# Kernel tuning notes

Measured on AMD Instinct MI355X. Metric: run time of the kernel, lower is better.

## Reference

```python
import jax, jax.numpy as jnp
import numpy as np

B, C, H, W = 8, 512, 64, 64
D = C // 8  # 64

def setup_inputs() -> dict:
    key = jax.random.key(0)
    ks = jax.random.split(key, 10)
    s = 0.02
    return {
        "x":  jax.random.normal(ks[0], (B, C, H, W), dtype=jnp.float32),
        "Wq": jax.random.normal(ks[1], (D, C), dtype=jnp.float32) * s,
        "bq": jnp.zeros((D,), dtype=jnp.float32),
        "Wk": jax.random.normal(ks[2], (D, C), dtype=jnp.float32) * s,
        "bk": jnp.zeros((D,), dtype=jnp.float32),
        "Wv": jax.random.normal(ks[3], (D, C), dtype=jnp.float32) * s,
        "bv": jnp.zeros((D,), dtype=jnp.float32),
        "Wo": jax.random.normal(ks[4], (C, D), dtype=jnp.float32) * s,
        "bo": jnp.zeros((C,), dtype=jnp.float32),
        "gamma": jnp.full((1,), 0.5, dtype=jnp.float32),
    }

def reference(x, Wq, bq, Wk, bk, Wv, bv, Wo, bo, gamma):
    b, c, h, w = x.shape
    n = h * w
    xf = x.reshape(b, c, n)                                   # (B, C, N)
    # 1x1 convs == channel matmuls (spectral_norm only reparametrizes the weight)
    q = jnp.einsum('dc,bcn->bnd', Wq, xf) + bq                # (B, N, D)
    k = jnp.einsum('dc,bcn->bdn', Wk, xf) + bk[:, None]       # (B, D, N)
    v = jnp.einsum('dc,bcn->bdn', Wv, xf) + bv[:, None]       # (B, D, N)
    # unscaled scores, softmax over key index (last dim)
    attn = jax.nn.softmax(jnp.einsum('bnd,bdm->bnm', q, k), axis=-1)  # (B, N, N)
    out = jnp.einsum('bdm,bnm->bdn', v, attn)                 # (B, D, N)
    out = jnp.einsum('cd,bdn->bcn', Wo, out) + bo[:, None]    # (B, C, N)
    return (out * gamma + xf).reshape(b, c, h, w)
```

## Files before the change

### kernel.cpp

```cpp
#include <hip/hip_runtime.h>
#include <hip/hip_bf16.h>

#define DEVFN __device__ __forceinline__

typedef __bf16 bf16x8 __attribute__((ext_vector_type(8)));
typedef float f32x4 __attribute__((ext_vector_type(4)));
typedef float float4_t __attribute__((ext_vector_type(4)));
typedef unsigned short ushort8_t __attribute__((ext_vector_type(8)));
typedef unsigned short ushort4_t __attribute__((ext_vector_type(4)));
typedef unsigned int uint4_t __attribute__((ext_vector_type(4)));

constexpr int Bd = 8, Cd = 512, Nd = 4096, Dd = 64;

DEVFN unsigned short f2bf(float f) {
    union { float f; unsigned int u; } v; v.f = f;
    unsigned int r = (v.u + 0x7FFFu + ((v.u >> 16) & 1u)) >> 16;
    return (unsigned short)r;
}

DEVFN unsigned int pack2(float a, float b) {
    __hip_bfloat162 h = __float22bfloat162_rn(make_float2(a, b));
    union { __hip_bfloat162 h; unsigned int u; } c; c.h = h;
    return c.u;
}

DEVFN bf16x8 ld_bf8(const unsigned short* p) {
    ushort8_t u = *(const ushort8_t*)p;
    return __builtin_bit_cast(bf16x8, u);
}

DEVFN f32x4 mfma16(bf16x8 a, bf16x8 b, f32x4 c) {
    return __builtin_amdgcn_mfma_f32_16x16x32_bf16(a, b, c, 0, 0, 0);
}

__global__ __launch_bounds__(256) void k_cvtw(
    const float* __restrict__ Wq, const float* __restrict__ Wk,
    const float* __restrict__ Wv, const float* __restrict__ Wo,
    unsigned short* __restrict__ w4)
{
    int i = blockIdx.x * 256 + threadIdx.x;
    w4[i]          = f2bf(Wq[i]);
    w4[32768 + i]  = f2bf(Wk[i]);
    w4[65536 + i]  = f2bf(Wv[i]);
    w4[98304 + i]  = f2bf(Wo[i]);
}

__global__ __launch_bounds__(256) void k_qkv(
    const float* __restrict__ x,
    const unsigned short* __restrict__ wq,
    const unsigned short* __restrict__ wk,
    const unsigned short* __restrict__ wv,
    const float* __restrict__ bq, const float* __restrict__ bk, const float* __restrict__ bv,
    unsigned short* __restrict__ q_nd, unsigned short* __restrict__ k_nd,
    unsigned short* __restrict__ v_dn)
{
    const int b   = blockIdx.y;
    const int n0  = blockIdx.x * 64;
    const int tid = threadIdx.x, wid = tid >> 6, l = tid & 63;
    const int lo  = l & 15, hi = l >> 4;
    const int n0w = n0 + wid * 16;
    const float* xb = x + (size_t)b * Cd * Nd;

    __shared__ unsigned short t_lds[4][16][72];
    __shared__ unsigned short vt_s[64][72];

    f32x4 accq[4] = {}, acck[4] = {}, accv[4] = {};

    for (int c0 = 0; c0 < Cd; c0 += 32) {
        ushort8_t ux;
        #pragma unroll
        for (int j = 0; j < 8; ++j)
            ux[j] = f2bf(xb[(size_t)(c0 + hi * 8 + j) * Nd + n0w + lo]);
        bf16x8 bx = __builtin_bit_cast(bf16x8, ux);
        #pragma unroll
        for (int ds = 0; ds < 4; ++ds) {
            const int wrow = (ds * 16 + lo) * Cd + c0 + hi * 8;
            accq[ds] = mfma16(ld_bf8(wq + wrow), bx, accq[ds]);
            acck[ds] = mfma16(ld_bf8(wk + wrow), bx, acck[ds]);
            accv[ds] = mfma16(ld_bf8(wv + wrow), bx, accv[ds]);
        }
    }

    const int row = l >> 2, dg = l & 3;

    #pragma unroll
    for (int ds = 0; ds < 4; ++ds) {
        ushort4_t u4;
        #pragma unroll
        for (int r = 0; r < 4; ++r) u4[r] = f2bf(accq[ds][r] + bq[ds*16 + hi*4 + r]);
        *(ushort4_t*)&t_lds[wid][lo][ds*16 + hi*4] = u4;
    }
    __syncthreads();
    {
        ushort8_t a0 = *(const ushort8_t*)&t_lds[wid][row][dg*16];
        ushort8_t a1 = *(const ushort8_t*)&t_lds[wid][row][dg*16 + 8];
        unsigned short* dst = q_nd + ((size_t)b * Nd + n0 + wid*16 + row) * 64 + dg*16;
        *(ushort8_t*)dst = a0; *(ushort8_t*)(dst + 8) = a1;
    }
    __syncthreads();

    #pragma unroll
    for (int ds = 0; ds < 4; ++ds) {
        ushort4_t u4;
        #pragma unroll
        for (int r = 0; r < 4; ++r) u4[r] = f2bf(acck[ds][r] + bk[ds*16 + hi*4 + r]);
        *(ushort4_t*)&t_lds[wid][lo][ds*16 + hi*4] = u4;
    }
    __syncthreads();
    {
        ushort8_t a0 = *(const ushort8_t*)&t_lds[wid][row][dg*16];
        ushort8_t a1 = *(const ushort8_t*)&t_lds[wid][row][dg*16 + 8];
        unsigned short* dst = k_nd + ((size_t)b * Nd + n0 + wid*16 + row) * 64 + dg*16;
        *(ushort8_t*)dst = a0; *(ushort8_t*)(dst + 8) = a1;
    }
    __syncthreads();

    #pragma unroll
    for (int ds = 0; ds < 4; ++ds) {
        #pragma unroll
        for (int r = 0; r < 4; ++r)
            vt_s[ds*16 + hi*4 + r][wid*16 + lo] = f2bf(accv[ds][r] + bv[ds*16 + hi*4 + r]);
    }
    __syncthreads();
    {
        const int d = tid >> 2, ng = tid & 3;
        ushort8_t a0 = *(const ushort8_t*)&vt_s[d][ng*16];
        ushort8_t a1 = *(const ushort8_t*)&vt_s[d][ng*16 + 8];
        unsigned short* dst = v_dn + ((size_t)b * Dd + d) * Nd + n0 + ng*16;
        *(ushort8_t*)dst = a0; *(ushort8_t*)(dst + 8) = a1;
    }
}

__global__ __launch_bounds__(256, 2) void k_attn(
    const unsigned short* __restrict__ q_nd,
    const unsigned short* __restrict__ k_nd,
    const unsigned short* __restrict__ v_dn,
    unsigned short* __restrict__ o_nd)
{
    const int bid = blockIdx.x;
    const int b   = bid & 7;
    const int n0  = (bid >> 3) * 64;
    const int tid = threadIdx.x, wid = tid >> 6, l = tid & 63;
    const int lo  = l & 15, hi = l >> 4;
    const int lsw = lo & 7;
    const int qh  = wid >> 1;
    const int kh  = wid & 1;
    const int wk0 = kh * 32;

    __shared__ unsigned short k_tiles[2][64 * 64];
    __shared__ unsigned short v_tiles[2][64 * 64];
    __shared__ float red_acc[2][2][4][256];
    __shared__ float red_l[2][2][16];

    const unsigned short* qb = q_nd + (size_t)b * Nd * Dd;
    const unsigned short* kb = k_nd + (size_t)b * Nd * Dd;
    const unsigned short* vb = v_dn + (size_t)b * Dd * Nd;

    bf16x8 aq[2][2];
    #pragma unroll
    for (int qs = 0; qs < 2; ++qs)
        #pragma unroll
        for (int kc = 0; kc < 2; ++kc)
            aq[qs][kc] = ld_bf8(qb + (size_t)(n0 + qh*32 + qs*16 + lo) * 64 + kc*32 + hi*8);

    f32x4 acc[2][4] = {};
    float l_p[2] = {0.f, 0.f};

    const int sr = tid >> 3, ss = tid & 7;
    const int kwsl = (ss ^ (sr & 7)) * 8;
    const int vkh = ss >> 2, vsl = ss & 3, vms = vsl >> 1;
    const int vg0 = vkh * 4 + ((2 * vsl) & 3);
    const int vg1 = vkh * 4 + ((2 * vsl + 1) & 3);
    const int vsw = sr & 7;
    ushort8_t kr0, kr1, vr0, vr1;

    auto gload = [&](int t) {
        const size_t m1 = (size_t)t * 64;
        kr0 = *(const ushort8_t*)(kb + (m1 + sr) * 64 + ss * 8);
        kr1 = *(const ushort8_t*)(kb + (m1 + 32 + sr) * 64 + ss * 8);
        vr0 = *(const ushort8_t*)(vb + (size_t)sr * Nd + m1 + ss * 8);
        vr1 = *(const ushort8_t*)(vb + (size_t)(32 + sr) * Nd + m1 + ss * 8);
    };
    auto dswrite = [&](int buf) {
        unsigned short* kt = k_tiles[buf];
        unsigned short* vt = v_tiles[buf];
        *(ushort8_t*)(kt + sr * 64 + kwsl)        = kr0;
        *(ushort8_t*)(kt + (32 + sr) * 64 + kwsl) = kr1;
        ushort4_t a0 = __builtin_shufflevector(vr0, vr0, 0, 1, 2, 3);
        ushort4_t a1 = __builtin_shufflevector(vr0, vr0, 4, 5, 6, 7);
        ushort4_t b0 = __builtin_shufflevector(vr1, vr1, 0, 1, 2, 3);
        ushort4_t b1 = __builtin_shufflevector(vr1, vr1, 4, 5, 6, 7);
        *(ushort4_t*)(vt + sr * 64 + (vg0 ^ vsw) * 8 + vms * 4)        = a0;
        *(ushort4_t*)(vt + sr * 64 + (vg1 ^ vsw) * 8 + vms * 4)        = a1;
        *(ushort4_t*)(vt + (32 + sr) * 64 + (vg0 ^ vsw) * 8 + vms * 4) = b0;
        *(ushort4_t*)(vt + (32 + sr) * 64 + (vg1 ^ vsw) * 8 + vms * 4) = b1;
    };

    auto compute = [&](int buf) {
        const unsigned short* kt = k_tiles[buf];
        const unsigned short* vt = v_tiles[buf];
        f32x4 s[2][2] = {};
        #pragma unroll
        for (int ms = 0; ms < 2; ++ms) {
            #pragma unroll
            for (int kc = 0; kc < 2; ++kc) {
                bf16x8 kf = ld_bf8(kt + (wk0 + ms*16 + lo) * 64 + (((kc*4 + hi) ^ lsw) * 8));
                #pragma unroll
                for (int qs = 0; qs < 2; ++qs)
                    s[qs][ms] = mfma16(kf, aq[qs][kc], s[qs][ms]);
            }
        }
        bf16x8 vf[4];
        #pragma unroll
        for (int ds = 0; ds < 4; ++ds)
            vf[ds] = ld_bf8(vt + (ds*16 + lo) * 64 + (((kh*4 + hi) ^ lsw) * 8));
        #pragma unroll
        for (int qs = 0; qs < 2; ++qs) {
            float p[2][4];
            #pragma unroll
            for (int ms = 0; ms < 2; ++ms)
                #pragma unroll
                for (int r = 0; r < 4; ++r)
                    p[ms][r] = __expf(s[qs][ms][r]);
            l_p[qs] += ((p[0][0] + p[0][1]) + (p[0][2] + p[0][3]))
                     + ((p[1][0] + p[1][1]) + (p[1][2] + p[1][3]));
            uint4_t w;
            w[0] = pack2(p[0][0], p[0][1]);
            w[1] = pack2(p[0][2], p[0][3]);
            w[2] = pack2(p[1][0], p[1][1]);
            w[3] = pack2(p[1][2], p[1][3]);
            bf16x8 apf = __builtin_bit_cast(bf16x8, w);
            #pragma unroll
            for (int ds = 0; ds < 4; ++ds)
                acc[qs][ds] = mfma16(apf, vf[ds], acc[qs][ds]);
        }
    };

    constexpr int NT = Nd / 64;
    gload(0);
    dswrite(0);
    __syncthreads();
    for (int t = 0; t < NT; ++t) {
        const int cur = t & 1;
        if (t + 1 < NT) gload(t + 1);
        __builtin_amdgcn_sched_barrier(0);
        compute(cur);
        if (t + 1 < NT) dswrite(cur ^ 1);
        __syncthreads();
    }

    float lh[2];
    #pragma unroll
    for (int qs = 0; qs < 2; ++qs) {
        float ps = l_p[qs];
        ps += __shfl_xor(ps, 16, 64);
        ps += __shfl_xor(ps, 32, 64);
        lh[qs] = ps;
    }
    if (kh == 1) {
        #pragma unroll
        for (int qs = 0; qs < 2; ++qs) {
            #pragma unroll
            for (int ds = 0; ds < 4; ++ds)
                *(f32x4*)&red_acc[qh][qs][ds][l * 4] = acc[qs][ds];
            red_l[qh][qs][lo] = lh[qs];
        }
    }
    __syncthreads();
    if (kh == 0) {
        #pragma unroll
        for (int qs = 0; qs < 2; ++qs) {
            #pragma unroll
            for (int ds = 0; ds < 4; ++ds)
                acc[qs][ds] += *(const f32x4*)&red_acc[qh][qs][ds][l * 4];
            float l_tot = lh[qs] + red_l[qh][qs][lo];
            #pragma unroll
            for (int r = 0; r < 4; ++r) {
                float lq = __shfl(l_tot, hi * 4 + r, 16);
                float rl = 1.0f / lq;
                #pragma unroll
                for (int ds = 0; ds < 4; ++ds) {
                    float o = acc[qs][ds][r] * rl;
                    o_nd[((size_t)b * Nd + n0 + qh*32 + qs*16 + hi*4 + r) * 64 + ds*16 + lo] = f2bf(o);
                }
            }
        }
    }
}

__global__ __launch_bounds__(256) void k_oproj(
    const unsigned short* __restrict__ o_nd,
    const unsigned short* __restrict__ wo,
    const float* __restrict__ bo,
    const float* __restrict__ gamma,
    const float* __restrict__ x,
    float* __restrict__ out)
{
    const int b   = blockIdx.y;
    const int n0  = blockIdx.x * 64;
    const int tid = threadIdx.x, wid = tid >> 6, l = tid & 63;
    const int lo  = l & 15, hi = l >> 4;
    const int n0w = n0 + wid * 16;
    const float g = gamma[0];

    bf16x8 ao[2];
    #pragma unroll
    for (int kc = 0; kc < 2; ++kc)
        ao[kc] = ld_bf8(o_nd + ((size_t)b * Nd + n0w + lo) * 64 + kc*32 + hi*8);

    for (int ct = 0; ct < 32; ++ct) {
        f32x4 acc = {};
        #pragma unroll
        for (int kc = 0; kc < 2; ++kc) {
            bf16x8 bw = ld_bf8(wo + (ct*16 + lo) * 64 + kc*32 + hi*8);
            acc = mfma16(ao[kc], bw, acc);
        }
        const int c = ct*16 + lo;
        const float bc = bo[c];
        const size_t base = ((size_t)b * Cd + c) * Nd + n0w + hi*4;
        float4_t xv = *(const float4_t*)(x + base);
        float4_t ov;
        #pragma unroll
        for (int r = 0; r < 4; ++r) ov[r] = g * (acc[r] + bc) + xv[r];
        *(float4_t*)(out + base) = ov;
    }
}

extern "C" void kernel_launch(void* const* d_in, const int* in_sizes, int n_in,
                              void* d_out, int out_size, void* d_ws, size_t ws_size,
                              hipStream_t stream) {
    (void)in_sizes; (void)n_in; (void)out_size; (void)ws_size;
    const float* x  = (const float*)d_in[0];
    const float* Wq = (const float*)d_in[1];
    const float* bq = (const float*)d_in[2];
    const float* Wk = (const float*)d_in[3];
    const float* bk = (const float*)d_in[4];
    const float* Wv = (const float*)d_in[5];
    const float* bv = (const float*)d_in[6];
    const float* Wo = (const float*)d_in[7];
    const float* bo = (const float*)d_in[8];
    const float* gm = (const float*)d_in[9];
    float* out = (float*)d_out;

    unsigned short* w4   = (unsigned short*)d_ws;
    unsigned short* q_nd = w4 + 131072;
    unsigned short* k_nd = q_nd + (size_t)Bd * Nd * Dd;
    unsigned short* v_dn = k_nd + (size_t)Bd * Nd * Dd;
    unsigned short* o_nd = v_dn + (size_t)Bd * Nd * Dd;

    k_cvtw<<<128, 256, 0, stream>>>(Wq, Wk, Wv, Wo, w4);
    dim3 g1(Nd / 64, Bd);
    k_qkv<<<g1, 256, 0, stream>>>(x, w4, w4 + 32768, w4 + 65536, bq, bk, bv, q_nd, k_nd, v_dn);
    k_attn<<<512, 256, 0, stream>>>(q_nd, k_nd, v_dn, o_nd);
    k_oproj<<<g1, 256, 0, stream>>>(o_nd, w4 + 98304, bo, gm, x, out);
}
```

Baseline: 151.3 us.

## Restructure QKV projection with coalesced x staging through double-buffered LDS

The QKV projection kernel now stages x tiles with vectorized float4 coalesced loads, converts them to bf16 into a double-buffered LDS tile, and prefetches the next channel chunk while computing the current one. Previously each lane did strided scalar global loads of x. Work is split across waves by token sub-tile and output half, each wave holding 6 accumulators. Tiles shrink to 32 tokens per block, with launch bounds raised for occupancy. Epilogue writes go straight to global memory without LDS transposes, so q and k stores become scattered 2-byte writes, which may cost write efficiency.

```diff
diff --git a/kernel.cpp b/kernel.cpp
--- a/kernel.cpp
+++ b/kernel.cpp
@@ -45,7 +45,7 @@
     w4[98304 + i]  = f2bf(Wo[i]);
 }
 
-__global__ __launch_bounds__(256) void k_qkv(
+__global__ __launch_bounds__(256, 4) void k_qkv(
     const float* __restrict__ x,
     const unsigned short* __restrict__ wq,
     const unsigned short* __restrict__ wk,
@@ -55,79 +55,77 @@
     unsigned short* __restrict__ v_dn)
 {
     const int b   = blockIdx.y;
-    const int n0  = blockIdx.x * 64;
+    const int n0  = blockIdx.x * 32;
     const int tid = threadIdx.x, wid = tid >> 6, l = tid & 63;
     const int lo  = l & 15, hi = l >> 4;
-    const int n0w = n0 + wid * 16;
+    const int ns  = wid >> 1;
+    const int oh  = wid & 1;
     const float* xb = x + (size_t)b * Cd * Nd;
 
-    __shared__ unsigned short t_lds[4][16][72];
-    __shared__ unsigned short vt_s[64][72];
-
-    f32x4 accq[4] = {}, acck[4] = {}, accv[4] = {};
-
-    for (int c0 = 0; c0 < Cd; c0 += 32) {
-        ushort8_t ux;
-        #pragma unroll
-        for (int j = 0; j < 8; ++j)
-            ux[j] = f2bf(xb[(size_t)(c0 + hi * 8 + j) * Nd + n0w + lo]);
-        bf16x8 bx = __builtin_bit_cast(bf16x8, ux);
-        #pragma unroll
-        for (int ds = 0; ds < 4; ++ds) {
-            const int wrow = (ds * 16 + lo) * Cd + c0 + hi * 8;
-            accq[ds] = mfma16(ld_bf8(wq + wrow), bx, accq[ds]);
-            acck[ds] = mfma16(ld_bf8(wk + wrow), bx, acck[ds]);
-            accv[ds] = mfma16(ld_bf8(wv + wrow), bx, accv[ds]);
-        }
-    }
-
-    const int row = l >> 2, dg = l & 3;
+    __shared__ unsigned short xt[2][32][72];
+
+    f32x4 acc[6] = {};
+
+    const int scr = tid >> 3, snf = tid & 7;
+    float4_t xr0, xr1;
+
+    auto gload = [&](int t) {
+        const int c0 = t * 64;
+        xr0 = *(const float4_t*)(xb + (size_t)(c0 + scr)      * Nd + n0 + snf * 4);
+        xr1 = *(const float4_t*)(xb + (size_t)(c0 + 32 + scr) * Nd + n0 + snf * 4);
+    };
+    auto dswrite = [&](int buf) {
+        #pragma unroll
+        for (int i = 0; i < 4; ++i) {
+            xt[buf][snf * 4 + i][scr]      = f2bf(xr0[i]);
+            xt[buf][snf * 4 + i][32 + scr] = f2bf(xr1[i]);
+        }
+    };
+    auto compute = [&](int buf, int t) {
+        #pragma unroll
+        for (int kk = 0; kk < 2; ++kk) {
+            const int c0 = t * 64 + kk * 32;
+            bf16x8 af = ld_bf8(&xt[buf][ns * 16 + lo][kk * 32 + hi * 8]);
+            #pragma unroll
+            for (int j = 0; j < 6; ++j) {
+                const int dt  = oh + 2 * j;
+                const unsigned short* wmat = (dt < 4) ? wq : (dt < 8) ? wk : wv;
+                const int d0  = (dt & 3) * 16;
+                bf16x8 bf = ld_bf8(wmat + (d0 + lo) * Cd + c0 + hi * 8);
+                acc[j] = mfma16(af, bf, acc[j]);
+            }
+        }
+    };
+
+    gload(0);
+    dswrite(0);
+    __syncthreads();
+    for (int t = 0; t < 8; ++t) {
+        const int cur = t & 1;
+        if (t + 1 < 8) gload(t + 1);
+        __builtin_amdgcn_sched_barrier(0);
+        compute(cur, t);
+        if (t + 1 < 8) dswrite(cur ^ 1);
+        __syncthreads();
+    }
 
     #pragma unroll
-    for (int ds = 0; ds < 4; ++ds) {
-        ushort4_t u4;
-        #pragma unroll
-        for (int r = 0; r < 4; ++r) u4[r] = f2bf(accq[ds][r] + bq[ds*16 + hi*4 + r]);
-        *(ushort4_t*)&t_lds[wid][lo][ds*16 + hi*4] = u4;
-    }
-    __syncthreads();
-    {
-        ushort8_t a0 = *(const ushort8_t*)&t_lds[wid][row][dg*16];
-        ushort8_t a1 = *(const ushort8_t*)&t_lds[wid][row][dg*16 + 8];
-        unsigned short* dst = q_nd + ((size_t)b * Nd + n0 + wid*16 + row) * 64 + dg*16;
-        *(ushort8_t*)dst = a0; *(ushort8_t*)(dst + 8) = a1;
-    }
-    __syncthreads();
-
-    #pragma unroll
-    for (int ds = 0; ds < 4; ++ds) {
-        ushort4_t u4;
-        #pragma unroll
-        for (int r = 0; r < 4; ++r) u4[r] = f2bf(acck[ds][r] + bk[ds*16 + hi*4 + r]);
-        *(ushort4_t*)&t_lds[wid][lo][ds*16 + hi*4] = u4;
-    }
-    __syncthreads();
-    {
-        ushort8_t a0 = *(const ushort8_t*)&t_lds[wid][row][dg*16];
-        ushort8_t a1 = *(const ushort8_t*)&t_lds[wid][row][dg*16 + 8];
-        unsigned short* dst = k_nd + ((size_t)b * Nd + n0 + wid*16 + row) * 64 + dg*16;
-        *(ushort8_t*)dst = a0; *(ushort8_t*)(dst + 8) = a1;
-    }
-    __syncthreads();
-
-    #pragma unroll
-    for (int ds = 0; ds < 4; ++ds) {
-        #pragma unroll
-        for (int r = 0; r < 4; ++r)
-            vt_s[ds*16 + hi*4 + r][wid*16 + lo] = f2bf(accv[ds][r] + bv[ds*16 + hi*4 + r]);
-    }
-    __syncthreads();
-    {
-        const int d = tid >> 2, ng = tid & 3;
-        ushort8_t a0 = *(const ushort8_t*)&vt_s[d][ng*16];
-        ushort8_t a1 = *(const ushort8_t*)&vt_s[d][ng*16 + 8];
-        unsigned short* dst = v_dn + ((size_t)b * Dd + d) * Nd + n0 + ng*16;
-        *(ushort8_t*)dst = a0; *(ushort8_t*)(dst + 8) = a1;
+    for (int j = 0; j < 6; ++j) {
+        const int dt  = oh + 2 * j;
+        const int mat = dt >> 2, d0 = (dt & 3) * 16;
+        const float bia = (mat == 0 ? bq : mat == 1 ? bk : bv)[d0 + lo];
+        if (mat < 2) {
+            unsigned short* dst = (mat == 0 ? q_nd : k_nd)
+                + ((size_t)b * Nd + n0 + ns * 16 + hi * 4) * 64 + d0 + lo;
+            #pragma unroll
+            for (int r = 0; r < 4; ++r)
+                dst[(size_t)r * 64] = f2bf(acc[j][r] + bia);
+        } else {
+            ushort4_t u;
+            #pragma unroll
+            for (int r = 0; r < 4; ++r) u[r] = f2bf(acc[j][r] + bia);
+            *(ushort4_t*)(v_dn + ((size_t)b * Dd + d0 + lo) * Nd + n0 + ns * 16 + hi * 4) = u;
+        }
     }
 }
 
@@ -349,8 +347,9 @@
     unsigned short* o_nd = v_dn + (size_t)Bd * Nd * Dd;
 
     k_cvtw<<<128, 256, 0, stream>>>(Wq, Wk, Wv, Wo, w4);
+    dim3 gq(Nd / 32, Bd);
+    k_qkv<<<gq, 256, 0, stream>>>(x, w4, w4 + 32768, w4 + 65536, bq, bk, bv, q_nd, k_nd, v_dn);
+    k_attn<<<512, 256, 0, stream>>>(q_nd, k_nd, v_dn, o_nd);
     dim3 g1(Nd / 64, Bd);
-    k_qkv<<<g1, 256, 0, stream>>>(x, w4, w4 + 32768, w4 + 65536, bq, bk, bv, q_nd, k_nd, v_dn);
-    k_attn<<<512, 256, 0, stream>>>(q_nd, k_nd, v_dn, o_nd);
     k_oproj<<<g1, 256, 0, stream>>>(o_nd, w4 + 98304, bo, gm, x, out);
 }
```

Result: slower. 228.6 us (+51.1%).
